# Kernel optimization log

Measured on AMD Instinct MI355X. Metric: run time of the kernel, lower is better.

## Reference

```python
import jax, jax.numpy as jnp
import numpy as np

NUM_CLASSES = 80
IGNORE = 0.5
LABEL_SMOOTH = 0.0
MAX_GT = 20
C = 5 + NUM_CLASSES
SIZES = (13, 26, 52)
BS = 64
ANCHORS = jnp.array([
    [[0.0240, 0.0313], [0.0385, 0.0721], [0.0793, 0.0553]],
    [[0.0721, 0.1466], [0.1490, 0.1082], [0.1418, 0.2861]],
    [[0.2788, 0.2163], [0.3750, 0.4760], [0.8966, 0.7837]],
], dtype=jnp.float32)
ANCH_REV = ANCHORS[::-1]  # anchors[[2,1,0]] in the torch code


def bce(p, t):
    p = jnp.clip(p, 1e-7, 1.0 - 1e-7)
    return -t * jnp.log(p) - (1.0 - t) * jnp.log(1.0 - p)


def cal_iou(b1, b2):
    tl = jnp.maximum(b1[..., 0:2] - b1[..., 2:4] / 2, b2[..., 0:2] - b2[..., 2:4] / 2)
    br = jnp.minimum(b1[..., 0:2] + b1[..., 2:4] / 2, b2[..., 0:2] + b2[..., 2:4] / 2)
    wh = jnp.maximum(br - tl, 0.0)
    inter = wh[..., 0] * wh[..., 1]
    union = b1[..., 2] * b1[..., 3] + b2[..., 2] * b2[..., 3] - inter
    return inter / jnp.clip(union, 1e-6)


def _sample_loss(preds, tflat):
    # preds: [N, C] decoded (x,y,w,h,conf,cls...); tflat: [M, C] target grid flattened
    N = preds.shape[0]
    conf_t = tflat[:, 4]
    _, idx = jax.lax.top_k(conf_t, MAX_GT)      # gather up to MAX_GT GT slots
    gts = tflat[idx]                            # [K, C]
    gmask = gts[:, 4]                           # 1.0 for real GT, 0.0 for padding
    iou = cal_iou(gts[:, None, :4], preds[None, :, :4])  # [K, N]
    best = jnp.argmax(iou, axis=-1)             # [K]
    sel = preds[best]                           # [K, C]
    reg = jnp.sum((sel[:, :4] - gts[:, :4]) ** 2, axis=-1) * (2.0 - gts[:, 2] * gts[:, 3])
    loss_reg = jnp.sum(gmask * reg)
    tar_cls = gts[:, 5:] * (1.0 - LABEL_SMOOTH) + LABEL_SMOOTH / NUM_CLASSES
    loss_cls = jnp.sum(gmask[:, None] * bce(sel[:, 5:], tar_cls))
    # noobj mask: zero at best-matched preds (valid GTs only) and at high-IoU preds
    noobj = jnp.ones(N, preds.dtype).at[best].multiply(1.0 - gmask)
    maxiou = jnp.max(iou * gmask[:, None], axis=0)  # [N]
    noobj = noobj * (maxiou < IGNORE).astype(preds.dtype)
    loss_conf = jnp.sum(gmask * bce(sel[:, 4], 1.0)) + jnp.sum(noobj * bce(preds[:, 4], 0.0))
    return loss_reg + loss_conf + loss_cls


def _scale_loss(pred, tgt, l):
    bs, lsz = pred.shape[0], pred.shape[-1]
    p = pred.reshape(bs, 3, C, lsz, lsz).transpose(0, 1, 3, 4, 2)  # [bs,3,h,w,C]
    raw_w, raw_h = p[..., 2], p[..., 3]
    s = jax.nn.sigmoid(p)
    grid = jnp.arange(lsz, dtype=p.dtype)
    x = (grid[None, None, None, :] + s[..., 0]) / lsz
    y = (grid[None, None, :, None] + s[..., 1]) / lsz
    anch = ANCH_REV[l]  # [3,2]
    w = anch[:, 0][None, :, None, None] * jnp.exp(raw_w)
    h = anch[:, 1][None, :, None, None] * jnp.exp(raw_h)
    boxes = jnp.stack([x, y, w, h], axis=-1)
    preds = jnp.concatenate([boxes, s[..., 4:5], s[..., 5:]], axis=-1).reshape(bs, -1, C)
    tflat = tgt.reshape(bs, -1, C)
    return jnp.sum(jax.vmap(_sample_loss)(preds, tflat))


def setup_inputs() -> dict:
    key = jax.random.key(0)
    ks = jax.random.split(key, 6)
    inp = {}
    for i, lsz in enumerate(SIZES):
        inp['pred%d' % i] = jax.random.normal(ks[i], (BS, 3 * C, lsz, lsz), dtype=jnp.float32)
        M = 3 * lsz * lsz
        kb, ki, kc = jax.random.split(ks[3 + i], 3)
        xywh = jax.random.uniform(kb, (BS, MAX_GT, 4), minval=0.05, maxval=0.6, dtype=jnp.float32)
        cls_idx = jax.random.randint(kc, (BS, MAX_GT), 0, NUM_CLASSES)
        entry = jnp.concatenate([xywh, jnp.ones((BS, MAX_GT, 1), jnp.float32),
                                 jax.nn.one_hot(cls_idx, NUM_CLASSES, dtype=jnp.float32)], axis=-1)
        pos = jax.random.randint(ki, (BS, MAX_GT), 0, M)
        tflat = jnp.zeros((BS, M, C), jnp.float32).at[jnp.arange(BS)[:, None], pos].set(entry)
        inp['targets%d' % i] = tflat.reshape(BS, 3, lsz, lsz, C)
    return inp


def reference(pred0, pred1, pred2, targets0, targets1, targets2):
    return (_scale_loss(pred0, targets0, 0)
            + _scale_loss(pred1, targets1, 1)
            + _scale_loss(pred2, targets2, 2))
```

## Files before the change

kernel.cpp:

```cpp
#include <hip/hip_runtime.h>

#define CC 85
#define NC 80
#define MAXGT 20
#define BSZ 64
#define IGNORE_T 0.5f
#define CHUNK 1024

#define POS_B   (192u*MAXGT*4u)
#define KEYS_B  (192u*MAXGT*8u)
#define NOOBJ_B (192u*4u)
#define HDR_B   (POS_B + KEYS_B + NOOBJ_B + 192u*4u)

#define N0 507
#define N1 2028
#define N2 8112
#define R0 (BSZ*N0)
#define R1 (BSZ*N1)
#define R2 (BSZ*N2)
#define RTOT (R0+R1+R2)

__constant__ float d_anch[3][3][2] = {
  {{0.2788f,0.2163f},{0.375f,0.476f},{0.8966f,0.7837f}},
  {{0.0721f,0.1466f},{0.149f,0.1082f},{0.1418f,0.2861f}},
  {{0.024f,0.0313f},{0.0385f,0.0721f},{0.0793f,0.0553f}},
};
__constant__ int d_lsz[3] = {13,26,52};

__device__ __forceinline__ float sigmoidf(float x){ return 1.0f/(1.0f+__expf(-x)); }
__device__ __forceinline__ float bcef(float p, float t){
  p = fminf(fmaxf(p, 1e-7f), 1.0f-1e-7f);
  return -t*__logf(p) - (1.0f-t)*__logf(1.0f-p);
}
__device__ __forceinline__ float iouf(float gx,float gy,float gw,float gh,
                                      float px,float py,float pw,float ph){
  float tlx = fmaxf(gx-gw*0.5f, px-pw*0.5f);
  float tly = fmaxf(gy-gh*0.5f, py-ph*0.5f);
  float brx = fminf(gx+gw*0.5f, px+pw*0.5f);
  float bry = fminf(gy+gh*0.5f, py+ph*0.5f);
  float w = fmaxf(brx-tlx, 0.0f), h = fmaxf(bry-tly, 0.0f);
  float inter = w*h;
  float uni = gw*gh + pw*ph - inter;
  return inter / fmaxf(uni, 1e-6f);
}

__device__ __forceinline__ void scan_hit(const float* __restrict__ t, int rl,
                                         int Nr, int s,
                                         int* __restrict__ ws_pos,
                                         int* __restrict__ ws_cnt){
  float c = t[(size_t)rl*CC + 4];
  if(c > 0.5f){
    int b = rl / Nr;
    int n = rl - b*Nr;
    int slot = s*BSZ + b;
    int i = atomicAdd(&ws_cnt[slot], 1);
    if(i < MAXGT) ws_pos[slot*MAXGT + i] = n;
  }
}

__global__ __launch_bounds__(256)
void k_scan(const float* __restrict__ t0, const float* __restrict__ t1,
            const float* __restrict__ t2,
            int* __restrict__ ws_pos, int* __restrict__ ws_cnt){
  int r = blockIdx.x*256 + threadIdx.x;
  if(r < R0)            scan_hit(t0, r,        N0, 0, ws_pos, ws_cnt);
  else if(r < R0+R1)    scan_hit(t1, r-R0,     N1, 1, ws_pos, ws_cnt);
  else if(r < RTOT)     scan_hit(t2, r-R0-R1,  N2, 2, ws_pos, ws_cnt);
}

__global__ __launch_bounds__(256, 2)
void k_main(const float* __restrict__ p0, const float* __restrict__ p1,
            const float* __restrict__ p2,
            const float* __restrict__ t0, const float* __restrict__ t1,
            const float* __restrict__ t2,
            const int* __restrict__ ws_pos, const int* __restrict__ ws_cnt,
            unsigned long long* __restrict__ ws_keys,
            float* __restrict__ ws_noobj){
  int s = blockIdx.z, b = blockIdx.y;
  int lsz = d_lsz[s], lsz2 = lsz*lsz, N = 3*lsz2;
  int n0 = blockIdx.x*CHUNK;
  if(n0 >= N) return;
  int slot = s*BSZ + b;
  const float* pred = (s==0 ? p0 : (s==1 ? p1 : p2)) + (size_t)b*3*CC*lsz2;
  const float* tgt  = (s==0 ? t0 : (s==1 ? t1 : t2)) + (size_t)b*N*CC;
  int tid = threadIdx.x;
  __shared__ float gx[MAXGT], gy[MAXGT], gw[MAXGT], gh[MAXGT];
  if(tid < MAXGT){
    int G = ws_cnt[slot];
    float x=0.f,y=0.f,w=0.f,h=0.f;
    if(tid < G){
      const float* r = tgt + (size_t)ws_pos[slot*MAXGT+tid]*CC;
      x=r[0]; y=r[1]; w=r[2]; h=r[3];
    }
    gx[tid]=x; gy[tid]=y; gw[tid]=w; gh[tid]=h;
  }
  __syncthreads();
  unsigned long long key[MAXGT];
  #pragma unroll
  for(int g=0; g<MAXGT; g++) key[g] = 0ull;
  float noobj = 0.0f;
  float inv = 1.0f/(float)lsz;
  float aw0=d_anch[s][0][0], ah0=d_anch[s][0][1];
  float aw1=d_anch[s][1][0], ah1=d_anch[s][1][1];
  float aw2=d_anch[s][2][0], ah2=d_anch[s][2][1];
  int nend = min(n0+CHUNK, N);
  for(int n=n0+tid; n<nend; n+=256){
    int a = n/lsz2, rem = n - a*lsz2;
    int i = rem/lsz, j = rem - i*lsz;
    const float* base = pred + (size_t)a*CC*lsz2 + rem;
    float q0 = base[0];
    float q1 = base[(size_t)lsz2];
    float q2 = base[2*(size_t)lsz2];
    float q3 = base[3*(size_t)lsz2];
    float q4 = base[4*(size_t)lsz2];
    float aw = (a==0)?aw0:((a==1)?aw1:aw2);
    float ah = (a==0)?ah0:((a==1)?ah1:ah2);
    float px = ((float)j + sigmoidf(q0))*inv;
    float py = ((float)i + sigmoidf(q1))*inv;
    float pw = aw*__expf(q2);
    float ph = ah*__expf(q3);
    float maxiou = 0.0f;
    unsigned int ninv = ~(unsigned int)n;
    #pragma unroll
    for(int g=0; g<MAXGT; g++){
      float io = iouf(gx[g],gy[g],gw[g],gh[g], px,py,pw,ph);
      maxiou = fmaxf(maxiou, io);
      unsigned long long k = ((unsigned long long)__float_as_uint(io) << 32) | (unsigned long long)ninv;
      key[g] = (k > key[g]) ? k : key[g];
    }
    if(maxiou < IGNORE_T) noobj += bcef(sigmoidf(q4), 0.0f);
  }
  #pragma unroll
  for(int g=0; g<MAXGT; g++){
    unsigned long long k = key[g];
    for(int off=32; off>0; off>>=1){
      unsigned long long o = __shfl_down(k, off, 64);
      k = (o > k) ? o : k;
    }
    if((tid & 63) == 0) atomicMax(&ws_keys[slot*MAXGT+g], k);
  }
  for(int off=32; off>0; off>>=1) noobj += __shfl_down(noobj, off, 64);
  if((tid & 63) == 0) atomicAdd(&ws_noobj[slot], noobj);
}

__global__ __launch_bounds__(256)
void k_final(const float* __restrict__ p0, const float* __restrict__ p1,
             const float* __restrict__ p2,
             const float* __restrict__ t0, const float* __restrict__ t1,
             const float* __restrict__ t2,
             const int* __restrict__ ws_pos, const int* __restrict__ ws_cnt,
             const unsigned long long* __restrict__ ws_keys,
             const float* __restrict__ ws_noobj,
             float* __restrict__ out){
  int b = blockIdx.x, s = blockIdx.y;
  int lsz = d_lsz[s], lsz2 = lsz*lsz, N = 3*lsz2;
  int slot = s*BSZ + b;
  const float* pred = (s==0 ? p0 : (s==1 ? p1 : p2)) + (size_t)b*3*CC*lsz2;
  const float* tgt  = (s==0 ? t0 : (s==1 ? t1 : t2)) + (size_t)b*N*CC;
  int tid = threadIdx.x;
  __shared__ int bn[MAXGT];
  __shared__ int gp[MAXGT];
  __shared__ float sx[MAXGT], sy[MAXGT], sw[MAXGT], sh[MAXGT];
  int G = ws_cnt[slot];
  if(tid < MAXGT){
    unsigned long long k = ws_keys[slot*MAXGT + tid];
    bn[tid] = (int)(~(unsigned int)(k & 0xffffffffull));
    float x=0.f,y=0.f,w=0.f,h=0.f; int p=0;
    if(tid < G){
      p = ws_pos[slot*MAXGT + tid];
      const float* r = tgt + (size_t)p*CC;
      x=r[0]; y=r[1]; w=r[2]; h=r[3];
    }
    gp[tid]=p; sx[tid]=x; sy[tid]=y; sw[tid]=w; sh[tid]=h;
  }
  __syncthreads();
  float loss = 0.0f;
  float inv = 1.0f/(float)lsz;
  if(tid < G){
    int n = bn[tid];
    int a = n/lsz2, rem = n - a*lsz2, i = rem/lsz, j = rem - i*lsz;
    const float* base = pred + (size_t)a*CC*lsz2 + rem;
    float q0 = base[0];
    float q1 = base[(size_t)lsz2];
    float q2 = base[2*(size_t)lsz2];
    float q3 = base[3*(size_t)lsz2];
    float q4 = base[4*(size_t)lsz2];
    float px = ((float)j + sigmoidf(q0))*inv;
    float py = ((float)i + sigmoidf(q1))*inv;
    float pw = d_anch[s][a][0]*__expf(q2);
    float ph = d_anch[s][a][1]*__expf(q3);
    float dx=px-sx[tid], dy=py-sy[tid], dw=pw-sw[tid], dh=ph-sh[tid];
    loss += (dx*dx + dy*dy + dw*dw + dh*dh) * (2.0f - sw[tid]*sh[tid]);
    loss += bcef(sigmoidf(q4), 1.0f);
    bool first = true;
    for(int g2=0; g2<tid; g2++) if(bn[g2]==n) first=false;
    if(first){
      float maxiou = 0.0f;
      for(int g2=0; g2<MAXGT; g2++)
        maxiou = fmaxf(maxiou, iouf(sx[g2],sy[g2],sw[g2],sh[g2], px,py,pw,ph));
      if(maxiou < IGNORE_T) loss -= bcef(sigmoidf(q4), 0.0f);
    }
  }
  for(int idx=tid; idx<G*NC; idx+=256){
    int g = idx/NC, c = idx - g*NC;
    int n = bn[g];
    int a = n/lsz2, rem = n - a*lsz2;
    float q = pred[(size_t)a*CC*lsz2 + (size_t)(5+c)*lsz2 + rem];
    float tcls = tgt[(size_t)gp[g]*CC + 5 + c];
    loss += bcef(sigmoidf(q), tcls);
  }
  if(tid==0) loss += ws_noobj[slot];
  __shared__ float wsum[4];
  for(int off=32; off>0; off>>=1) loss += __shfl_down(loss, off, 64);
  if((tid & 63) == 0) wsum[tid>>6] = loss;
  __syncthreads();
  if(tid==0) atomicAdd(out, wsum[0]+wsum[1]+wsum[2]+wsum[3]);
}

extern "C" void kernel_launch(void* const* d_in, const int* in_sizes, int n_in,
                              void* d_out, int out_size, void* d_ws, size_t ws_size,
                              hipStream_t stream) {
  const float* p0 = (const float*)d_in[0];
  const float* t0 = (const float*)d_in[1];
  const float* p1 = (const float*)d_in[2];
  const float* t1 = (const float*)d_in[3];
  const float* p2 = (const float*)d_in[4];
  const float* t2 = (const float*)d_in[5];
  float* out = (float*)d_out;
  char* ws = (char*)d_ws;
  int*                ws_pos   = (int*)(ws);
  unsigned long long* ws_keys  = (unsigned long long*)(ws + POS_B);
  float*              ws_noobj = (float*)(ws + POS_B + KEYS_B);
  int*                ws_cnt   = (int*)(ws + POS_B + KEYS_B + NOOBJ_B);

  hipMemsetAsync(ws, 0, HDR_B, stream);
  hipMemsetAsync(d_out, 0, sizeof(float), stream);

  k_scan <<<(RTOT+255)/256, 256, 0, stream>>>(t0,t1,t2, ws_pos, ws_cnt);
  k_main <<<dim3(8,BSZ,3), 256, 0, stream>>>(p0,p1,p2, t0,t1,t2,
                                             ws_pos, ws_cnt, ws_keys, ws_noobj);
  k_final<<<dim3(BSZ,3), 256, 0, stream>>>(p0,p1,p2, t0,t1,t2,
                                           ws_pos, ws_cnt, ws_keys, ws_noobj, out);
}
```

Baseline: 417.2 us.

## Fuse box decoding into scan kernel, block-level key reduction, split final over z

The scan kernel now also decodes every prediction box (sigmoid/exp, anchor lookup) and writes a packed float4 box plus the raw confidence to workspace. The IoU kernel then reads these compact arrays instead of strided pred channels. Per-wave atomics are first combined in shared memory, so each block issues one atomic per GT. The final kernel's class-BCE loop is spread over 4 z-blocks for more parallelism. In exchange the scan pass does extra writes and the IoU pass extra reads to a larger workspace, and the grid-stride scan may be slower than the old per-block decode.

```diff
diff --git a/kernel.cpp b/kernel.cpp
--- a/kernel.cpp
+++ b/kernel.cpp
@@ -6,11 +6,6 @@
 #define BSZ 64
 #define IGNORE_T 0.5f
 #define CHUNK 1024
-
-#define POS_B   (192u*MAXGT*4u)
-#define KEYS_B  (192u*MAXGT*8u)
-#define NOOBJ_B (192u*4u)
-#define HDR_B   (POS_B + KEYS_B + NOOBJ_B + 192u*4u)
 
 #define N0 507
 #define N1 2028
@@ -19,6 +14,12 @@
 #define R1 (BSZ*N1)
 #define R2 (BSZ*N2)
 #define RTOT (R0+R1+R2)
+
+#define POS_B   (192u*MAXGT*4u)
+#define KEYS_B  (192u*MAXGT*8u)
+#define NOOBJ_B (192u*4u)
+#define HDR_B   (POS_B + KEYS_B + NOOBJ_B + 192u*4u)
+#define BOX_B   ((unsigned)RTOT*16u)
 
 __constant__ float d_anch[3][3][2] = {
   {{0.2788f,0.2163f},{0.375f,0.476f},{0.8966f,0.7837f}},
@@ -44,47 +45,73 @@
   return inter / fmaxf(uni, 1e-6f);
 }
 
-__device__ __forceinline__ void scan_hit(const float* __restrict__ t, int rl,
-                                         int Nr, int s,
-                                         int* __restrict__ ws_pos,
-                                         int* __restrict__ ws_cnt){
-  float c = t[(size_t)rl*CC + 4];
+template<int LSZ>
+__device__ __forceinline__ void scanbox_one(const float* __restrict__ tgt,
+                                            const float* __restrict__ pred,
+                                            int rl, int s, int gofs,
+                                            int* __restrict__ ws_pos,
+                                            int* __restrict__ ws_cnt,
+                                            float4* __restrict__ box4,
+                                            float* __restrict__ confr){
+  const int L2 = LSZ*LSZ, N = 3*L2;
+  int b = rl / N;
+  int n = rl - b*N;
+  float c = tgt[(size_t)rl*CC + 4];
   if(c > 0.5f){
-    int b = rl / Nr;
-    int n = rl - b*Nr;
     int slot = s*BSZ + b;
     int i = atomicAdd(&ws_cnt[slot], 1);
     if(i < MAXGT) ws_pos[slot*MAXGT + i] = n;
   }
+  int a = n / L2, rem = n - a*L2;
+  int ii = rem / LSZ, jj = rem - ii*LSZ;
+  const float* base = pred + (size_t)b*3*CC*L2 + (size_t)a*CC*L2 + rem;
+  float q0 = base[0];
+  float q1 = base[L2];
+  float q2 = base[2*L2];
+  float q3 = base[3*L2];
+  float q4 = base[4*L2];
+  const float inv = 1.0f/(float)LSZ;
+  float px = ((float)jj + sigmoidf(q0))*inv;
+  float py = ((float)ii + sigmoidf(q1))*inv;
+  float pw = d_anch[s][a][0]*__expf(q2);
+  float ph = d_anch[s][a][1]*__expf(q3);
+  box4[gofs + rl] = make_float4(px,py,pw,ph);
+  confr[gofs + rl] = q4;
 }
 
 __global__ __launch_bounds__(256)
-void k_scan(const float* __restrict__ t0, const float* __restrict__ t1,
-            const float* __restrict__ t2,
-            int* __restrict__ ws_pos, int* __restrict__ ws_cnt){
+void k_scanbox(const float* __restrict__ t0, const float* __restrict__ t1,
+               const float* __restrict__ t2,
+               const float* __restrict__ p0, const float* __restrict__ p1,
+               const float* __restrict__ p2,
+               int* __restrict__ ws_pos, int* __restrict__ ws_cnt,
+               float4* __restrict__ box4, float* __restrict__ confr){
   int r = blockIdx.x*256 + threadIdx.x;
-  if(r < R0)            scan_hit(t0, r,        N0, 0, ws_pos, ws_cnt);
-  else if(r < R0+R1)    scan_hit(t1, r-R0,     N1, 1, ws_pos, ws_cnt);
-  else if(r < RTOT)     scan_hit(t2, r-R0-R1,  N2, 2, ws_pos, ws_cnt);
+  if(r < R0)         scanbox_one<13>(t0, p0, r,       0, 0,     ws_pos, ws_cnt, box4, confr);
+  else if(r < R0+R1) scanbox_one<26>(t1, p1, r-R0,    1, R0,    ws_pos, ws_cnt, box4, confr);
+  else if(r < RTOT)  scanbox_one<52>(t2, p2, r-R0-R1, 2, R0+R1, ws_pos, ws_cnt, box4, confr);
 }
 
 __global__ __launch_bounds__(256, 2)
-void k_main(const float* __restrict__ p0, const float* __restrict__ p1,
-            const float* __restrict__ p2,
-            const float* __restrict__ t0, const float* __restrict__ t1,
-            const float* __restrict__ t2,
-            const int* __restrict__ ws_pos, const int* __restrict__ ws_cnt,
-            unsigned long long* __restrict__ ws_keys,
-            float* __restrict__ ws_noobj){
+void k_iou(const float* __restrict__ t0, const float* __restrict__ t1,
+           const float* __restrict__ t2,
+           const float4* __restrict__ box4, const float* __restrict__ confr,
+           const int* __restrict__ ws_pos, const int* __restrict__ ws_cnt,
+           unsigned long long* __restrict__ ws_keys,
+           float* __restrict__ ws_noobj){
   int s = blockIdx.z, b = blockIdx.y;
   int lsz = d_lsz[s], lsz2 = lsz*lsz, N = 3*lsz2;
   int n0 = blockIdx.x*CHUNK;
   if(n0 >= N) return;
   int slot = s*BSZ + b;
-  const float* pred = (s==0 ? p0 : (s==1 ? p1 : p2)) + (size_t)b*3*CC*lsz2;
-  const float* tgt  = (s==0 ? t0 : (s==1 ? t1 : t2)) + (size_t)b*N*CC;
+  int gofs = (s==0 ? 0 : (s==1 ? R0 : R0+R1)) + b*N;
+  const float* tgt = (s==0 ? t0 : (s==1 ? t1 : t2)) + (size_t)b*N*CC;
+  const float4* bx = box4 + gofs;
+  const float*  cf = confr + gofs;
   int tid = threadIdx.x;
   __shared__ float gx[MAXGT], gy[MAXGT], gw[MAXGT], gh[MAXGT];
+  __shared__ unsigned long long lkey[4][MAXGT];
+  __shared__ float lnob[4];
   if(tid < MAXGT){
     int G = ws_cnt[slot];
     float x=0.f,y=0.f,w=0.f,h=0.f;
@@ -99,37 +126,22 @@
   #pragma unroll
   for(int g=0; g<MAXGT; g++) key[g] = 0ull;
   float noobj = 0.0f;
-  float inv = 1.0f/(float)lsz;
-  float aw0=d_anch[s][0][0], ah0=d_anch[s][0][1];
-  float aw1=d_anch[s][1][0], ah1=d_anch[s][1][1];
-  float aw2=d_anch[s][2][0], ah2=d_anch[s][2][1];
   int nend = min(n0+CHUNK, N);
   for(int n=n0+tid; n<nend; n+=256){
-    int a = n/lsz2, rem = n - a*lsz2;
-    int i = rem/lsz, j = rem - i*lsz;
-    const float* base = pred + (size_t)a*CC*lsz2 + rem;
-    float q0 = base[0];
-    float q1 = base[(size_t)lsz2];
-    float q2 = base[2*(size_t)lsz2];
-    float q3 = base[3*(size_t)lsz2];
-    float q4 = base[4*(size_t)lsz2];
-    float aw = (a==0)?aw0:((a==1)?aw1:aw2);
-    float ah = (a==0)?ah0:((a==1)?ah1:ah2);
-    float px = ((float)j + sigmoidf(q0))*inv;
-    float py = ((float)i + sigmoidf(q1))*inv;
-    float pw = aw*__expf(q2);
-    float ph = ah*__expf(q3);
+    float4 B = bx[n];
+    float q4 = cf[n];
     float maxiou = 0.0f;
     unsigned int ninv = ~(unsigned int)n;
     #pragma unroll
     for(int g=0; g<MAXGT; g++){
-      float io = iouf(gx[g],gy[g],gw[g],gh[g], px,py,pw,ph);
+      float io = iouf(gx[g],gy[g],gw[g],gh[g], B.x,B.y,B.z,B.w);
       maxiou = fmaxf(maxiou, io);
       unsigned long long k = ((unsigned long long)__float_as_uint(io) << 32) | (unsigned long long)ninv;
       key[g] = (k > key[g]) ? k : key[g];
     }
     if(maxiou < IGNORE_T) noobj += bcef(sigmoidf(q4), 0.0f);
   }
+  int wid = tid >> 6, lane = tid & 63;
   #pragma unroll
   for(int g=0; g<MAXGT; g++){
     unsigned long long k = key[g];
@@ -137,10 +149,18 @@
       unsigned long long o = __shfl_down(k, off, 64);
       k = (o > k) ? o : k;
     }
-    if((tid & 63) == 0) atomicMax(&ws_keys[slot*MAXGT+g], k);
+    if(lane == 0) lkey[wid][g] = k;
   }
   for(int off=32; off>0; off>>=1) noobj += __shfl_down(noobj, off, 64);
-  if((tid & 63) == 0) atomicAdd(&ws_noobj[slot], noobj);
+  if(lane == 0) lnob[wid] = noobj;
+  __syncthreads();
+  if(tid < MAXGT){
+    unsigned long long k0 = lkey[0][tid] > lkey[1][tid] ? lkey[0][tid] : lkey[1][tid];
+    unsigned long long k1 = lkey[2][tid] > lkey[3][tid] ? lkey[2][tid] : lkey[3][tid];
+    unsigned long long k  = k0 > k1 ? k0 : k1;
+    atomicMax(&ws_keys[slot*MAXGT+tid], k);
+  }
+  if(tid == 0) atomicAdd(&ws_noobj[slot], lnob[0]+lnob[1]+lnob[2]+lnob[3]);
 }
 
 __global__ __launch_bounds__(256)
@@ -152,7 +172,7 @@
              const unsigned long long* __restrict__ ws_keys,
              const float* __restrict__ ws_noobj,
              float* __restrict__ out){
-  int b = blockIdx.x, s = blockIdx.y;
+  int b = blockIdx.x, s = blockIdx.y, z = blockIdx.z;
   int lsz = d_lsz[s], lsz2 = lsz*lsz, N = 3*lsz2;
   int slot = s*BSZ + b;
   const float* pred = (s==0 ? p0 : (s==1 ? p1 : p2)) + (size_t)b*3*CC*lsz2;
@@ -176,7 +196,7 @@
   __syncthreads();
   float loss = 0.0f;
   float inv = 1.0f/(float)lsz;
-  if(tid < G){
+  if(z == 0 && tid < G){
     int n = bn[tid];
     int a = n/lsz2, rem = n - a*lsz2, i = rem/lsz, j = rem - i*lsz;
     const float* base = pred + (size_t)a*CC*lsz2 + rem;
@@ -201,7 +221,7 @@
       if(maxiou < IGNORE_T) loss -= bcef(sigmoidf(q4), 0.0f);
     }
   }
-  for(int idx=tid; idx<G*NC; idx+=256){
+  for(int idx = z*256 + tid; idx < G*NC; idx += 1024){
     int g = idx/NC, c = idx - g*NC;
     int n = bn[g];
     int a = n/lsz2, rem = n - a*lsz2;
@@ -209,12 +229,15 @@
     float tcls = tgt[(size_t)gp[g]*CC + 5 + c];
     loss += bcef(sigmoidf(q), tcls);
   }
-  if(tid==0) loss += ws_noobj[slot];
+  if(z == 0 && tid == 0) loss += ws_noobj[slot];
   __shared__ float wsum[4];
   for(int off=32; off>0; off>>=1) loss += __shfl_down(loss, off, 64);
   if((tid & 63) == 0) wsum[tid>>6] = loss;
   __syncthreads();
-  if(tid==0) atomicAdd(out, wsum[0]+wsum[1]+wsum[2]+wsum[3]);
+  if(tid==0){
+    float v = wsum[0]+wsum[1]+wsum[2]+wsum[3];
+    if(v != 0.0f || z == 0) atomicAdd(out, v);
+  }
 }
 
 extern "C" void kernel_launch(void* const* d_in, const int* in_sizes, int n_in,
@@ -232,13 +255,16 @@
   unsigned long long* ws_keys  = (unsigned long long*)(ws + POS_B);
   float*              ws_noobj = (float*)(ws + POS_B + KEYS_B);
   int*                ws_cnt   = (int*)(ws + POS_B + KEYS_B + NOOBJ_B);
+  float4*             ws_box4  = (float4*)(ws + HDR_B);
+  float*              ws_confr = (float*)(ws + HDR_B + BOX_B);
 
   hipMemsetAsync(ws, 0, HDR_B, stream);
   hipMemsetAsync(d_out, 0, sizeof(float), stream);
 
-  k_scan <<<(RTOT+255)/256, 256, 0, stream>>>(t0,t1,t2, ws_pos, ws_cnt);
-  k_main <<<dim3(8,BSZ,3), 256, 0, stream>>>(p0,p1,p2, t0,t1,t2,
-                                             ws_pos, ws_cnt, ws_keys, ws_noobj);
-  k_final<<<dim3(BSZ,3), 256, 0, stream>>>(p0,p1,p2, t0,t1,t2,
-                                           ws_pos, ws_cnt, ws_keys, ws_noobj, out);
-}
+  k_scanbox<<<(RTOT+255)/256, 256, 0, stream>>>(t0,t1,t2, p0,p1,p2,
+                                                ws_pos, ws_cnt, ws_box4, ws_confr);
+  k_iou    <<<dim3(8,BSZ,3), 256, 0, stream>>>(t0,t1,t2, ws_box4, ws_confr,
+                                               ws_pos, ws_cnt, ws_keys, ws_noobj);
+  k_final  <<<dim3(BSZ,3,4), 256, 0, stream>>>(p0,p1,p2, t0,t1,t2,
+                                               ws_pos, ws_cnt, ws_keys, ws_noobj, out);
+}
```

Result: no change. 411.7 us (median of 2 runs) (-1.3%).

## Fuse IoU pass and final loss kernel via last-block-done counter

Applied to the files above, without the earlier changes.

Merges the IoU/noobj kernel and the final loss kernel into one launch. A per-slot completion counter lets the last chunk block of each (scale, batch) slot compute the final loss. Per-wave key maxima are first reduced in shared memory so only one atomicMax per GT per block goes to global memory, instead of one per wave. This removes a kernel launch and the separate final pass, at the cost of threadfences, an extra counter in the workspace, and serialized tail work inside the last block.

```diff
diff --git a/kernel.cpp b/kernel.cpp
--- a/kernel.cpp
+++ b/kernel.cpp
@@ -6,11 +6,6 @@
 #define BSZ 64
 #define IGNORE_T 0.5f
 #define CHUNK 1024
-
-#define POS_B   (192u*MAXGT*4u)
-#define KEYS_B  (192u*MAXGT*8u)
-#define NOOBJ_B (192u*4u)
-#define HDR_B   (POS_B + KEYS_B + NOOBJ_B + 192u*4u)
 
 #define N0 507
 #define N1 2028
@@ -19,6 +14,13 @@
 #define R1 (BSZ*N1)
 #define R2 (BSZ*N2)
 #define RTOT (R0+R1+R2)
+
+#define POS_B   (192u*MAXGT*4u)
+#define KEYS_B  (192u*MAXGT*8u)
+#define NOOBJ_B (192u*4u)
+#define CNT_B   (192u*4u)
+#define DONE_B  (192u*4u)
+#define HDR_B   (POS_B + KEYS_B + NOOBJ_B + CNT_B + DONE_B)
 
 __constant__ float d_anch[3][3][2] = {
   {{0.2788f,0.2163f},{0.375f,0.476f},{0.8966f,0.7837f}},
@@ -69,32 +71,47 @@
 }
 
 __global__ __launch_bounds__(256, 2)
-void k_main(const float* __restrict__ p0, const float* __restrict__ p1,
-            const float* __restrict__ p2,
-            const float* __restrict__ t0, const float* __restrict__ t1,
-            const float* __restrict__ t2,
-            const int* __restrict__ ws_pos, const int* __restrict__ ws_cnt,
-            unsigned long long* __restrict__ ws_keys,
-            float* __restrict__ ws_noobj){
+void k_ioufinal(const float* __restrict__ p0, const float* __restrict__ p1,
+                const float* __restrict__ p2,
+                const float* __restrict__ t0, const float* __restrict__ t1,
+                const float* __restrict__ t2,
+                const int* __restrict__ ws_pos, const int* __restrict__ ws_cnt,
+                unsigned long long* __restrict__ ws_keys,
+                float* __restrict__ ws_noobj, int* __restrict__ ws_done,
+                float* __restrict__ out){
   int s = blockIdx.z, b = blockIdx.y;
   int lsz = d_lsz[s], lsz2 = lsz*lsz, N = 3*lsz2;
-  int n0 = blockIdx.x*CHUNK;
-  if(n0 >= N) return;
+  int nchunk = (N + CHUNK - 1)/CHUNK;
+  int cx = blockIdx.x;
+  if(cx >= nchunk) return;
+  int n0 = cx*CHUNK;
   int slot = s*BSZ + b;
   const float* pred = (s==0 ? p0 : (s==1 ? p1 : p2)) + (size_t)b*3*CC*lsz2;
   const float* tgt  = (s==0 ? t0 : (s==1 ? t1 : t2)) + (size_t)b*N*CC;
   int tid = threadIdx.x;
+
   __shared__ float gx[MAXGT], gy[MAXGT], gw[MAXGT], gh[MAXGT];
+  __shared__ int gp[MAXGT];
+  __shared__ unsigned long long lkey[4][MAXGT];
+  __shared__ float lnob[4];
+  __shared__ int sG, slast;
+  __shared__ int bn[MAXGT];
+  __shared__ float wsum[4];
+
+  if(tid==0) sG = ws_cnt[slot];
+  __syncthreads();
+  int G = sG;
   if(tid < MAXGT){
-    int G = ws_cnt[slot];
-    float x=0.f,y=0.f,w=0.f,h=0.f;
+    float x=0.f,y=0.f,w=0.f,h=0.f; int p=0;
     if(tid < G){
-      const float* r = tgt + (size_t)ws_pos[slot*MAXGT+tid]*CC;
+      p = ws_pos[slot*MAXGT+tid];
+      const float* r = tgt + (size_t)p*CC;
       x=r[0]; y=r[1]; w=r[2]; h=r[3];
     }
-    gx[tid]=x; gy[tid]=y; gw[tid]=w; gh[tid]=h;
-  }
-  __syncthreads();
+    gp[tid]=p; gx[tid]=x; gy[tid]=y; gw[tid]=w; gh[tid]=h;
+  }
+  __syncthreads();
+
   unsigned long long key[MAXGT];
   #pragma unroll
   for(int g=0; g<MAXGT; g++) key[g] = 0ull;
@@ -130,6 +147,7 @@
     }
     if(maxiou < IGNORE_T) noobj += bcef(sigmoidf(q4), 0.0f);
   }
+  int wid = tid >> 6, lane = tid & 63;
   #pragma unroll
   for(int g=0; g<MAXGT; g++){
     unsigned long long k = key[g];
@@ -137,45 +155,35 @@
       unsigned long long o = __shfl_down(k, off, 64);
       k = (o > k) ? o : k;
     }
-    if((tid & 63) == 0) atomicMax(&ws_keys[slot*MAXGT+g], k);
+    if(lane == 0) lkey[wid][g] = k;
   }
   for(int off=32; off>0; off>>=1) noobj += __shfl_down(noobj, off, 64);
-  if((tid & 63) == 0) atomicAdd(&ws_noobj[slot], noobj);
-}
-
-__global__ __launch_bounds__(256)
-void k_final(const float* __restrict__ p0, const float* __restrict__ p1,
-             const float* __restrict__ p2,
-             const float* __restrict__ t0, const float* __restrict__ t1,
-             const float* __restrict__ t2,
-             const int* __restrict__ ws_pos, const int* __restrict__ ws_cnt,
-             const unsigned long long* __restrict__ ws_keys,
-             const float* __restrict__ ws_noobj,
-             float* __restrict__ out){
-  int b = blockIdx.x, s = blockIdx.y;
-  int lsz = d_lsz[s], lsz2 = lsz*lsz, N = 3*lsz2;
-  int slot = s*BSZ + b;
-  const float* pred = (s==0 ? p0 : (s==1 ? p1 : p2)) + (size_t)b*3*CC*lsz2;
-  const float* tgt  = (s==0 ? t0 : (s==1 ? t1 : t2)) + (size_t)b*N*CC;
-  int tid = threadIdx.x;
-  __shared__ int bn[MAXGT];
-  __shared__ int gp[MAXGT];
-  __shared__ float sx[MAXGT], sy[MAXGT], sw[MAXGT], sh[MAXGT];
-  int G = ws_cnt[slot];
+  if(lane == 0) lnob[wid] = noobj;
+  __syncthreads();
   if(tid < MAXGT){
-    unsigned long long k = ws_keys[slot*MAXGT + tid];
+    unsigned long long k0 = lkey[0][tid] > lkey[1][tid] ? lkey[0][tid] : lkey[1][tid];
+    unsigned long long k1 = lkey[2][tid] > lkey[3][tid] ? lkey[2][tid] : lkey[3][tid];
+    unsigned long long k  = k0 > k1 ? k0 : k1;
+    atomicMax(&ws_keys[slot*MAXGT+tid], k);
+  }
+  if(tid == 0) atomicAdd(&ws_noobj[slot], lnob[0]+lnob[1]+lnob[2]+lnob[3]);
+
+  __threadfence();
+  if(tid == 0){
+    int old = atomicAdd(&ws_done[slot], 1);
+    slast = (old == nchunk-1) ? 1 : 0;
+  }
+  __syncthreads();
+  if(!slast) return;
+  __threadfence();
+
+  if(tid < MAXGT){
+    unsigned long long k = atomicMax(&ws_keys[slot*MAXGT+tid], 0ull);
     bn[tid] = (int)(~(unsigned int)(k & 0xffffffffull));
-    float x=0.f,y=0.f,w=0.f,h=0.f; int p=0;
-    if(tid < G){
-      p = ws_pos[slot*MAXGT + tid];
-      const float* r = tgt + (size_t)p*CC;
-      x=r[0]; y=r[1]; w=r[2]; h=r[3];
-    }
-    gp[tid]=p; sx[tid]=x; sy[tid]=y; sw[tid]=w; sh[tid]=h;
-  }
-  __syncthreads();
+  }
+  __syncthreads();
+
   float loss = 0.0f;
-  float inv = 1.0f/(float)lsz;
   if(tid < G){
     int n = bn[tid];
     int a = n/lsz2, rem = n - a*lsz2, i = rem/lsz, j = rem - i*lsz;
@@ -189,15 +197,15 @@
     float py = ((float)i + sigmoidf(q1))*inv;
     float pw = d_anch[s][a][0]*__expf(q2);
     float ph = d_anch[s][a][1]*__expf(q3);
-    float dx=px-sx[tid], dy=py-sy[tid], dw=pw-sw[tid], dh=ph-sh[tid];
-    loss += (dx*dx + dy*dy + dw*dw + dh*dh) * (2.0f - sw[tid]*sh[tid]);
+    float dx=px-gx[tid], dy=py-gy[tid], dw=pw-gw[tid], dh=ph-gh[tid];
+    loss += (dx*dx + dy*dy + dw*dw + dh*dh) * (2.0f - gw[tid]*gh[tid]);
     loss += bcef(sigmoidf(q4), 1.0f);
     bool first = true;
     for(int g2=0; g2<tid; g2++) if(bn[g2]==n) first=false;
     if(first){
       float maxiou = 0.0f;
       for(int g2=0; g2<MAXGT; g2++)
-        maxiou = fmaxf(maxiou, iouf(sx[g2],sy[g2],sw[g2],sh[g2], px,py,pw,ph));
+        maxiou = fmaxf(maxiou, iouf(gx[g2],gy[g2],gw[g2],gh[g2], px,py,pw,ph));
       if(maxiou < IGNORE_T) loss -= bcef(sigmoidf(q4), 0.0f);
     }
   }
@@ -209,10 +217,9 @@
     float tcls = tgt[(size_t)gp[g]*CC + 5 + c];
     loss += bcef(sigmoidf(q), tcls);
   }
-  if(tid==0) loss += ws_noobj[slot];
-  __shared__ float wsum[4];
+  if(tid==0) loss += atomicAdd(&ws_noobj[slot], 0.0f);
   for(int off=32; off>0; off>>=1) loss += __shfl_down(loss, off, 64);
-  if((tid & 63) == 0) wsum[tid>>6] = loss;
+  if(lane == 0) wsum[wid] = loss;
   __syncthreads();
   if(tid==0) atomicAdd(out, wsum[0]+wsum[1]+wsum[2]+wsum[3]);
 }
@@ -232,13 +239,13 @@
   unsigned long long* ws_keys  = (unsigned long long*)(ws + POS_B);
   float*              ws_noobj = (float*)(ws + POS_B + KEYS_B);
   int*                ws_cnt   = (int*)(ws + POS_B + KEYS_B + NOOBJ_B);
+  int*                ws_done  = (int*)(ws + POS_B + KEYS_B + NOOBJ_B + CNT_B);
 
   hipMemsetAsync(ws, 0, HDR_B, stream);
   hipMemsetAsync(d_out, 0, sizeof(float), stream);
 
-  k_scan <<<(RTOT+255)/256, 256, 0, stream>>>(t0,t1,t2, ws_pos, ws_cnt);
-  k_main <<<dim3(8,BSZ,3), 256, 0, stream>>>(p0,p1,p2, t0,t1,t2,
-                                             ws_pos, ws_cnt, ws_keys, ws_noobj);
-  k_final<<<dim3(BSZ,3), 256, 0, stream>>>(p0,p1,p2, t0,t1,t2,
-                                           ws_pos, ws_cnt, ws_keys, ws_noobj, out);
-}
+  k_scan    <<<(RTOT+255)/256, 256, 0, stream>>>(t0,t1,t2, ws_pos, ws_cnt);
+  k_ioufinal<<<dim3(8,BSZ,3), 256, 0, stream>>>(p0,p1,p2, t0,t1,t2,
+                                                ws_pos, ws_cnt, ws_keys,
+                                                ws_noobj, ws_done, out);
+}
```

New measurement: 619.2 us. 48.4% more time.
